# Performance work log

Measured on AMD Instinct MI355X. Metric: run time of the kernel, lower is better.

The kernel has to match this reference:

```python
import jax, jax.numpy as jnp
import numpy as np

B, L, V, D, C, R = 8, 2048, 32000, 512, 64, 64
NBLK = 2           # n_layers - 1
H = 2 * D          # stem hidden dim
STD = 0.02


def _ln(x, w, b):
    m = x.mean(-1, keepdims=True)
    v = ((x - m) ** 2).mean(-1, keepdims=True)
    return (x - m) / jnp.sqrt(v + 1e-5) * w + b


def setup_inputs() -> dict:
    key = jax.random.key(0)
    ks = jax.random.split(key, 16)
    n = lambda k, shp: jax.random.normal(k, shp, dtype=jnp.float32) * STD
    return {
        "token_ids": jax.random.randint(ks[0], (B, L), 0, V),
        "tok_emb": n(ks[1], (V, D)),
        "pos_emb": n(ks[2], (L, D)),
        "stem_ln_w": jnp.ones((NBLK, D), jnp.float32),
        "stem_ln_b": jnp.zeros((NBLK, D), jnp.float32),
        "stem_w1": n(ks[3], (NBLK, D, H)),
        "stem_b1": jnp.zeros((NBLK, H), jnp.float32),
        "stem_w2": n(ks[4], (NBLK, H, D)),
        "stem_b2": jnp.zeros((NBLK, D), jnp.float32),
        "role_ln_w": jnp.ones((D,), jnp.float32),
        "role_ln_b": jnp.zeros((D,), jnp.float32),
        "Wa": n(ks[5], (D, R)),
        "Wb": n(ks[6], (D, R)),
        "Wc": n(ks[7], (D, R)),
        "class_a": n(ks[8], (C, R)),
        "class_b": n(ks[9], (C, R)),
        "class_c": n(ks[10], (C, R)),
        "query_ln_w": jnp.ones((D,), jnp.float32),
        "query_ln_b": jnp.zeros((D,), jnp.float32),
        "Wq": n(ks[11], (D, C)),
        "bq": jnp.zeros((C,), jnp.float32),
    }


def reference(token_ids, tok_emb, pos_emb, stem_ln_w, stem_ln_b, stem_w1,
              stem_b1, stem_w2, stem_b2, role_ln_w, role_ln_b, Wa, Wb, Wc,
              class_a, class_b, class_c, query_ln_w, query_ln_b, Wq, bq):
    seq_len = token_ids.shape[1]
    x = tok_emb[token_ids] + pos_emb[:seq_len][None, :, :]  # [B,L,D]
    for i in range(NBLK):
        h = _ln(x, stem_ln_w[i], stem_ln_b[i])
        h = jax.nn.gelu(h @ stem_w1[i] + stem_b1[i], approximate=False)
        x = x + h @ stem_w2[i] + stem_b2[i]
    prefix = _ln(x[:, :-1], role_ln_w, role_ln_b)  # [B,L-1,D]
    a = jnp.tanh(prefix @ Wa)
    b = jnp.tanh(prefix @ Wb)
    c = jnp.tanh(prefix @ Wc)
    ua = jnp.einsum('blr,cr->blc', a, class_a)  # [B,L-1,C]
    ub = jnp.einsum('blr,cr->blc', b, class_b)
    uc = jnp.einsum('blr,cr->blc', c, class_c)
    # exact ordered-triplet sum  sum_{i<j<k} ua_i * ub_j * uc_k  via exclusive cumsums
    prefA = jnp.cumsum(ua, axis=1) - ua            # sum_{i<j} ua_i
    t = ub * prefA
    prefT = jnp.cumsum(t, axis=1) - t              # sum_{j<k} ub_j * prefA_j
    s = (uc * prefT).sum(axis=1)                   # [B,C]
    Lp = max(seq_len - 1, 1)
    denom = max(Lp * (Lp - 1) * (Lp - 2) / 6.0, 1.0)
    q = _ln(x[:, -1], query_ln_w, query_ln_b)
    return s / denom + q @ Wq + bq
```

## Files before the change

### kernel.cpp

```cpp
#include <hip/hip_runtime.h>

#define NROWS 16384
#define LSEQ  2048
#define NB    8

typedef short v8s __attribute__((ext_vector_type(8)));
typedef float v4f __attribute__((ext_vector_type(4)));

__device__ __forceinline__ unsigned short f2bf(float f) {
    unsigned int u = __float_as_uint(f);
    return (unsigned short)((u + 0x7fffu + ((u >> 16) & 1u)) >> 16);
}
__device__ __forceinline__ float bf2f(unsigned short u) {
    return __uint_as_float(((unsigned int)u) << 16);
}

__device__ __forceinline__ void glds16(const void* g, void* l) {
    __builtin_amdgcn_global_load_lds(
        (__attribute__((address_space(1))) void*)g,
        (__attribute__((address_space(3))) void*)l,
        16, 0, 0);
}

__device__ __forceinline__ float fast_gelu(float v) {
    float z = fabsf(v) * 0.70710678118654752f;
    float t = __builtin_amdgcn_rcpf(1.0f + 0.3275911f * z);
    float poly = t * (0.254829592f + t * (-0.284496736f + t * (1.421413741f +
                 t * (-1.453152027f + t * 1.061405429f))));
    float erfz = 1.0f - poly * __expf(-z * z);
    float er = copysignf(erfz, v);
    return 0.5f * v * (1.0f + er);
}
__device__ __forceinline__ float fast_tanh(float y) {
    float e = __expf(2.0f * y);
    return (e - 1.0f) * __builtin_amdgcn_rcpf(e + 1.0f);
}

__device__ __forceinline__ long swizzled_row(int b, int wave) {
    int T = (b & 7) + (((b >> 3) & 15) << 3);
    int chunk = b >> 7;
    return (long)T * 128 + chunk * 4 + wave;
}

__global__ __launch_bounds__(256) void setup_kernel(
        const int* __restrict__ ids,
        const float* __restrict__ tok, const float* __restrict__ pos,
        const float* __restrict__ g0, const float* __restrict__ b0,
        unsigned short* __restrict__ x, unsigned short* __restrict__ hl,
        const float* __restrict__ w1, const float* __restrict__ w2,
        const float* __restrict__ wa, const float* __restrict__ wb, const float* __restrict__ wc,
        const float* __restrict__ ca, const float* __restrict__ cb, const float* __restrict__ cc,
        unsigned short* __restrict__ w1T, unsigned short* __restrict__ w2T,
        unsigned short* __restrict__ wabcT, unsigned short* __restrict__ clsb) {
    int blk = blockIdx.x;
    int t = threadIdx.x;
    if (blk < 4096) {
        int wave = t >> 6, lane = t & 63;
        long row = swizzled_row(blk, wave);
        int l = (int)(row & (LSEQ - 1));
        int id = ids[row];
        int d = lane * 8;
        float4 t0 = *(const float4*)(tok + (size_t)id * 512 + d);
        float4 t1 = *(const float4*)(tok + (size_t)id * 512 + d + 4);
        float4 p0 = *(const float4*)(pos + (size_t)l * 512 + d);
        float4 p1 = *(const float4*)(pos + (size_t)l * 512 + d + 4);
        float a[8] = {t0.x + p0.x, t0.y + p0.y, t0.z + p0.z, t0.w + p0.w,
                      t1.x + p1.x, t1.y + p1.y, t1.z + p1.z, t1.w + p1.w};
        unsigned int xp[4];
        #pragma unroll
        for (int i = 0; i < 4; ++i)
            xp[i] = (unsigned int)f2bf(a[2 * i]) | ((unsigned int)f2bf(a[2 * i + 1]) << 16);
        *(uint4*)(x + row * 512 + d) = *(uint4*)xp;
        float s = 0.f, s2 = 0.f;
        #pragma unroll
        for (int i = 0; i < 8; ++i) { s += a[i]; s2 += a[i] * a[i]; }
        #pragma unroll
        for (int o = 32; o > 0; o >>= 1) { s += __shfl_down(s, o); s2 += __shfl_down(s2, o); }
        s = __shfl(s, 0); s2 = __shfl(s2, 0);
        float m = s * (1.0f / 512.0f);
        float rinv = 1.0f / sqrtf(s2 * (1.0f / 512.0f) - m * m + 1e-5f);
        float4 ga = *(const float4*)(g0 + d), gb = *(const float4*)(g0 + d + 4);
        float4 ba = *(const float4*)(b0 + d), bb2 = *(const float4*)(b0 + d + 4);
        float gg[8] = {ga.x, ga.y, ga.z, ga.w, gb.x, gb.y, gb.z, gb.w};
        float bb[8] = {ba.x, ba.y, ba.z, ba.w, bb2.x, bb2.y, bb2.z, bb2.w};
        unsigned int hp[4];
        #pragma unroll
        for (int i = 0; i < 4; ++i) {
            unsigned short lo = f2bf((a[2 * i]     - m) * rinv * gg[2 * i]     + bb[2 * i]);
            unsigned short hi = f2bf((a[2 * i + 1] - m) * rinv * gg[2 * i + 1] + bb[2 * i + 1]);
            hp[i] = (unsigned int)lo | ((unsigned int)hi << 16);
        }
        *(uint4*)(hl + row * 512 + d) = *(uint4*)hp;
    } else if (blk < 6240) {
        int id = blk - 4096;
        int tx = t & 31, ty = t >> 5;
        const float* in; unsigned short* out; int R, C, bx, by, ldo;
        if (id < 1024) {
            int l = id >> 9, r = id & 511;
            in = w1 + l * 524288; out = w1T + l * 524288;
            R = 512; C = 1024; bx = r & 31; by = r >> 5; ldo = 512;
        } else if (id < 2048) {
            int l = (id - 1024) >> 9, r = (id - 1024) & 511;
            in = w2 + l * 524288; out = w2T + l * 524288;
            R = 1024; C = 512; bx = r & 15; by = r >> 4; ldo = 1024;
        } else {
            int g = (id - 2048) >> 5, r = (id - 2048) & 31;
            in = (g == 0) ? wa : (g == 1) ? wb : wc;
            out = wabcT + g * 32768;
            R = 512; C = 64; bx = r & 1; by = r >> 1; ldo = 512;
        }
        __shared__ unsigned short tile[32][33];
        int c0 = bx * 32, r0 = by * 32;
        for (int i = ty; i < 32; i += 8) {
            int r = r0 + i, c = c0 + tx;
            tile[i][tx] = (r < R && c < C) ? f2bf(in[(size_t)r * C + c]) : (unsigned short)0;
        }
        __syncthreads();
        for (int i = ty; i < 32; i += 8) {
            int c = c0 + i, r = r0 + tx;
            if (r < R && c < C) out[(size_t)c * ldo + r] = tile[tx][i];
        }
    } else {
        int g = blk - 6240;
        const float* src = (g == 0) ? ca : (g == 1) ? cb : cc;
        unsigned short* dst = clsb + g * 4096;
        for (int i = t; i < 4096; i += 256) dst[i] = f2bf(src[i]);
    }
}

__global__ __launch_bounds__(256) void ln_kernel(const unsigned short* __restrict__ x,
        const float* __restrict__ g, const float* __restrict__ b,
        unsigned short* __restrict__ out) {
    int wave = threadIdx.x >> 6, lane = threadIdx.x & 63;
    long row = swizzled_row(blockIdx.x, wave);
    int d = lane * 8;
    uint4 xp = *(const uint4*)(x + row * 512 + d);
    const unsigned int* xw = (const unsigned int*)&xp;
    float a[8];
    #pragma unroll
    for (int i = 0; i < 4; ++i) {
        a[2 * i]     = bf2f((unsigned short)(xw[i] & 0xffff));
        a[2 * i + 1] = bf2f((unsigned short)(xw[i] >> 16));
    }
    float s = 0.f, s2 = 0.f;
    #pragma unroll
    for (int i = 0; i < 8; ++i) { s += a[i]; s2 += a[i] * a[i]; }
    #pragma unroll
    for (int o = 32; o > 0; o >>= 1) { s += __shfl_down(s, o); s2 += __shfl_down(s2, o); }
    s = __shfl(s, 0); s2 = __shfl(s2, 0);
    float m = s * (1.0f / 512.0f);
    float rinv = 1.0f / sqrtf(s2 * (1.0f / 512.0f) - m * m + 1e-5f);
    float4 g0 = *(const float4*)(g + d), g1 = *(const float4*)(g + d + 4);
    float4 b0 = *(const float4*)(b + d), b1 = *(const float4*)(b + d + 4);
    float gg[8] = {g0.x, g0.y, g0.z, g0.w, g1.x, g1.y, g1.z, g1.w};
    float bb[8] = {b0.x, b0.y, b0.z, b0.w, b1.x, b1.y, b1.z, b1.w};
    unsigned int hp[4];
    #pragma unroll
    for (int i = 0; i < 4; ++i) {
        unsigned short lo = f2bf((a[2 * i]     - m) * rinv * gg[2 * i]     + bb[2 * i]);
        unsigned short hi = f2bf((a[2 * i + 1] - m) * rinv * gg[2 * i + 1] + bb[2 * i + 1]);
        hp[i] = (unsigned int)lo | ((unsigned int)hi << 16);
    }
    *(uint4*)(out + row * 512 + d) = *(uint4*)hp;
}

#define EPI_GELU_BF16  0
#define EPI_RES_BF16   1

template <int EPI, int BN>
__global__ __launch_bounds__(512, 1) void gemm_8p(
        const unsigned short* __restrict__ A, int lda,
        const unsigned short* __restrict__ BT, int ldb,
        const float* __restrict__ bias,
        const unsigned short* __restrict__ xres,
        unsigned short* __restrict__ Cout, int ldc, int K) {
    constexpr int NFC = BN / 64;
    constexpr int FCH = NFC / 2;
    constexpr int NLB = BN / 128;
    constexpr int BH  = BN / 2;
    __shared__ unsigned short Ab[2][2][128 * 64] __attribute__((aligned(16)));
    __shared__ unsigned short Bb[2][2][BH * 64] __attribute__((aligned(16)));
    const int t = threadIdx.x;
    const int lane = t & 63, w = t >> 6;
    const int quad = lane >> 4, l16 = lane & 15;
    const int wmh = w >> 2;
    const int wn  = w & 3;
    const int bhalf = wn >> 1, bbase = (wn & 1) * (BN / 4);
    const long tileM = (long)blockIdx.x * 256;
    const long tileN = (long)blockIdx.y * BN;

    const int rl = lane >> 3;
    const int cl = ((lane & 7) ^ rl) * 8;

    const unsigned short* pa[2][2];
    #pragma unroll
    for (int h = 0; h < 2; ++h)
        #pragma unroll
        for (int q = 0; q < 2; ++q)
            pa[h][q] = A + (tileM + h * 128 + w * 16 + q * 8 + rl) * (size_t)lda + cl;
    const unsigned short* pb[2][2];
    #pragma unroll
    for (int h = 0; h < 2; ++h) {
        if constexpr (NLB == 2) {
            #pragma unroll
            for (int q = 0; q < 2; ++q)
                pb[h][q] = BT + (tileN + h * BH + w * 16 + q * 8 + rl) * (size_t)ldb + cl;
        } else {
            pb[h][0] = BT + (tileN + h * BH + w * 8 + rl) * (size_t)ldb + cl;
        }
    }
    int kA = 0, kB = 0;

    auto stageA = [&](int buf, int h) {
        glds16(pa[h][0] + kA, &Ab[buf][h][(w * 2 + 0) * 512]);
        glds16(pa[h][1] + kA, &Ab[buf][h][(w * 2 + 1) * 512]);
    };
    auto stageB = [&](int buf, int h) {
        if constexpr (NLB == 2) {
            glds16(pb[h][0] + kB, &Bb[buf][h][(w * 2 + 0) * 512]);
            glds16(pb[h][1] + kB, &Bb[buf][h][(w * 2 + 1) * 512]);
        } else {
            glds16(pb[h][0] + kB, &Bb[buf][h][w * 512]);
        }
    };

    const int xl = l16 & 7;
    const int ak0 = l16 * 64 + (((quad    ) ^ xl) * 8);
    const int ak1 = l16 * 64 + (((quad + 4) ^ xl) * 8);

    stageA(0, 0); stageA(0, 1); kA = 64;
    stageB(0, 0); stageB(0, 1); kB = 64;
    stageB(1, 0); stageB(1, 1); kB = 128;

    v4f acc[8][NFC] = {};
    const int nt = K >> 6;

    asm volatile("s_waitcnt vmcnt(%0)" :: "i"(2 * NLB) : "memory");
    __builtin_amdgcn_s_barrier();

    for (int tt = 0; tt < nt; ++tt) {
        const int bi = tt & 1;
        const unsigned short* Ah = &Ab[bi][wmh][0];
        const unsigned short* Bh = &Bb[bi][bhalf][bbase * 64];
        v8s af[4][2], bf[NFC][2];

        #pragma unroll
        for (int fr = 0; fr < 4; ++fr) {
            af[fr][0] = *(const v8s*)(Ah + fr * 1024 + ak0);
            af[fr][1] = *(const v8s*)(Ah + fr * 1024 + ak1);
        }
        #pragma unroll
        for (int fc = 0; fc < FCH; ++fc) {
            bf[fc][0] = *(const v8s*)(Bh + fc * 1024 + ak0);
            bf[fc][1] = *(const v8s*)(Bh + fc * 1024 + ak1);
        }
        if (tt + 1 < nt) stageA(bi ^ 1, 0);
        __builtin_amdgcn_s_barrier();
        asm volatile("s_waitcnt lgkmcnt(0)" ::: "memory");
        __builtin_amdgcn_s_setprio(1);
        #pragma unroll
        for (int fr = 0; fr < 4; ++fr)
            #pragma unroll
            for (int fc = 0; fc < FCH; ++fc) {
                acc[fr][fc] = __builtin_amdgcn_mfma_f32_16x16x32_bf16(bf[fc][0], af[fr][0], acc[fr][fc], 0, 0, 0);
                acc[fr][fc] = __builtin_amdgcn_mfma_f32_16x16x32_bf16(bf[fc][1], af[fr][1], acc[fr][fc], 0, 0, 0);
            }
        __builtin_amdgcn_s_setprio(0);
        __builtin_amdgcn_s_barrier();

        #pragma unroll
        for (int fc = FCH; fc < NFC; ++fc) {
            bf[fc][0] = *(const v8s*)(Bh + fc * 1024 + ak0);
            bf[fc][1] = *(const v8s*)(Bh + fc * 1024 + ak1);
        }
        if (tt + 1 < nt) stageA(bi ^ 1, 1);
        kA += 64;
        __builtin_amdgcn_s_barrier();
        asm volatile("s_waitcnt lgkmcnt(0)" ::: "memory");
        __builtin_amdgcn_s_setprio(1);
        #pragma unroll
        for (int fr = 0; fr < 4; ++fr)
            #pragma unroll
            for (int fc = FCH; fc < NFC; ++fc) {
                acc[fr][fc] = __builtin_amdgcn_mfma_f32_16x16x32_bf16(bf[fc][0], af[fr][0], acc[fr][fc], 0, 0, 0);
                acc[fr][fc] = __builtin_amdgcn_mfma_f32_16x16x32_bf16(bf[fc][1], af[fr][1], acc[fr][fc], 0, 0, 0);
            }
        __builtin_amdgcn_s_setprio(0);
        __builtin_amdgcn_s_barrier();

        #pragma unroll
        for (int fr = 0; fr < 4; ++fr) {
            af[fr][0] = *(const v8s*)(Ah + (fr + 4) * 1024 + ak0);
            af[fr][1] = *(const v8s*)(Ah + (fr + 4) * 1024 + ak1);
        }
        if (tt + 2 < nt) stageB(bi, 0);
        __builtin_amdgcn_s_barrier();
        asm volatile("s_waitcnt lgkmcnt(0)" ::: "memory");
        __builtin_amdgcn_s_setprio(1);
        #pragma unroll
        for (int fr = 0; fr < 4; ++fr)
            #pragma unroll
            for (int fc = 0; fc < FCH; ++fc) {
                acc[fr + 4][fc] = __builtin_amdgcn_mfma_f32_16x16x32_bf16(bf[fc][0], af[fr][0], acc[fr + 4][fc], 0, 0, 0);
                acc[fr + 4][fc] = __builtin_amdgcn_mfma_f32_16x16x32_bf16(bf[fc][1], af[fr][1], acc[fr + 4][fc], 0, 0, 0);
            }
        __builtin_amdgcn_s_setprio(0);
        __builtin_amdgcn_s_barrier();

        if (tt + 2 < nt) stageB(bi, 1);
        kB += 64;
        if (tt + 2 < nt)
            asm volatile("s_waitcnt vmcnt(%0)" :: "i"(2 * NLB) : "memory");
        else if (tt + 1 < nt)
            asm volatile("s_waitcnt vmcnt(0)" ::: "memory");
        __builtin_amdgcn_s_barrier();
        __builtin_amdgcn_s_setprio(1);
        #pragma unroll
        for (int fr = 0; fr < 4; ++fr)
            #pragma unroll
            for (int fc = FCH; fc < NFC; ++fc) {
                acc[fr + 4][fc] = __builtin_amdgcn_mfma_f32_16x16x32_bf16(bf[fc][0], af[fr][0], acc[fr + 4][fc], 0, 0, 0);
                acc[fr + 4][fc] = __builtin_amdgcn_mfma_f32_16x16x32_bf16(bf[fc][1], af[fr][1], acc[fr + 4][fc], 0, 0, 0);
            }
        __builtin_amdgcn_s_setprio(0);
        __builtin_amdgcn_s_barrier();
    }

    #pragma unroll
    for (int fr = 0; fr < 8; ++fr) {
        long m = tileM + wmh * 128 + fr * 16 + l16;
        #pragma unroll
        for (int fc = 0; fc < NFC; ++fc) {
            long n0 = tileN + wn * (BN / 4) + fc * 16 + quad * 4;
            float4 bi4 = *(const float4*)&bias[n0];
            const float* bip = (const float*)&bi4;
            unsigned short pk[4];
            if (EPI == EPI_GELU_BF16) {
                #pragma unroll
                for (int r = 0; r < 4; ++r)
                    pk[r] = f2bf(fast_gelu(acc[fr][fc][r] + bip[r]));
            } else {
                ushort4 xr4 = *(const ushort4*)&xres[m * ldc + n0];
                const unsigned short* xp = (const unsigned short*)&xr4;
                #pragma unroll
                for (int r = 0; r < 4; ++r)
                    pk[r] = f2bf(acc[fr][fc][r] + bip[r] + bf2f(xp[r]));
            }
            *(ushort4*)&Cout[m * ldc + n0] = *(ushort4*)pk;
        }
    }
}

__global__ __launch_bounds__(256) void tanh_class_kernel(
        const unsigned short* __restrict__ A,
        const unsigned short* __restrict__ WT,
        const unsigned short* __restrict__ cls,
        unsigned short* __restrict__ uu) {
    __shared__ unsigned short As[128][40] __attribute__((aligned(16)));
    __shared__ unsigned short Bs[64][40] __attribute__((aligned(16)));
    __shared__ unsigned short P[128 * 72] __attribute__((aligned(16)));
    const int t = threadIdx.x;
    const int lane = t & 63, wave = t >> 6;
    const int quad = lane >> 4, l16 = lane & 15;
    const int wm = (wave >> 1) * 64, wn = (wave & 1) * 32;
    const long tileM = (long)blockIdx.x * 128;
    const int g = blockIdx.y;
    const int arow = t >> 2, acol = (t & 3) * 8;

    const unsigned short* BT = WT + g * 32768;
    v8s cf[2][2];
    #pragma unroll
    for (int ks = 0; ks < 2; ++ks)
        #pragma unroll
        for (int j = 0; j < 2; ++j)
            cf[ks][j] = *(const v8s*)&cls[g * 4096 + (wn + j * 16 + l16) * 64 + ks * 32 + quad * 8];

    const unsigned short* gA0 = A + (tileM + arow) * 512 + acol;
    const unsigned short* gA1 = gA0 + 64 * 512;
    const unsigned short* gB0 = BT + arow * 512 + acol;

    v4f acc[4][2] = {};
    uint4 a0, a1, b0;
    a0 = *(const uint4*)gA0; a1 = *(const uint4*)gA1; gA0 += 32; gA1 += 32;
    b0 = *(const uint4*)gB0; gB0 += 32;
    *(uint4*)&As[arow][acol] = a0;
    *(uint4*)&As[arow + 64][acol] = a1;
    *(uint4*)&Bs[arow][acol] = b0;

    for (int kk = 0; kk < 16; ++kk) {
        __syncthreads();
        const bool more = kk < 15;
        if (more) {
            a0 = *(const uint4*)gA0; a1 = *(const uint4*)gA1; gA0 += 32; gA1 += 32;
            b0 = *(const uint4*)gB0; gB0 += 32;
        }
        v8s af[4], bfr[2];
        #pragma unroll
        for (int i = 0; i < 4; ++i) af[i] = *(const v8s*)&As[wm + i * 16 + l16][quad * 8];
        #pragma unroll
        for (int j = 0; j < 2; ++j) bfr[j] = *(const v8s*)&Bs[wn + j * 16 + l16][quad * 8];
        #pragma unroll
        for (int i = 0; i < 4; ++i)
            #pragma unroll
            for (int j = 0; j < 2; ++j)
                acc[i][j] = __builtin_amdgcn_mfma_f32_16x16x32_bf16(bfr[j], af[i], acc[i][j], 0, 0, 0);
        __syncthreads();
        if (more) {
            *(uint4*)&As[arow][acol] = a0;
            *(uint4*)&As[arow + 64][acol] = a1;
            *(uint4*)&Bs[arow][acol] = b0;
        }
    }

    #pragma unroll
    for (int i = 0; i < 4; ++i) {
        int m = wm + i * 16 + l16;
        #pragma unroll
        for (int j = 0; j < 2; ++j) {
            int n0 = wn + j * 16 + quad * 4;
            unsigned short pk[4];
            #pragma unroll
            for (int r = 0; r < 4; ++r) pk[r] = f2bf(fast_tanh(acc[i][j][r]));
            *(ushort4*)&P[m * 72 + n0] = *(ushort4*)pk;
        }
    }
    __syncthreads();

    v4f acc2[4][2] = {};
    #pragma unroll
    for (int ks = 0; ks < 2; ++ks) {
        v8s paf[4];
        #pragma unroll
        for (int i = 0; i < 4; ++i)
            paf[i] = *(const v8s*)&P[(wm + i * 16 + l16) * 72 + ks * 32 + quad * 8];
        #pragma unroll
        for (int i = 0; i < 4; ++i)
            #pragma unroll
            for (int j = 0; j < 2; ++j)
                acc2[i][j] = __builtin_amdgcn_mfma_f32_16x16x32_bf16(cf[ks][j], paf[i], acc2[i][j], 0, 0, 0);
    }

    #pragma unroll
    for (int i = 0; i < 4; ++i) {
        long m = tileM + wm + i * 16 + l16;
        #pragma unroll
        for (int j = 0; j < 2; ++j) {
            int c0 = wn + j * 16 + quad * 4;
            unsigned short pk[4];
            #pragma unroll
            for (int r = 0; r < 4; ++r) pk[r] = f2bf(acc2[i][j][r]);
            *(ushort4*)&uu[m * 192 + g * 64 + c0] = *(ushort4*)pk;
        }
    }
}

__global__ __launch_bounds__(64) void scan_part_kernel(const unsigned short* __restrict__ u,
                                                       float* __restrict__ part) {
    int b = blockIdx.x, seg = blockIdx.y;
    int c = threadIdx.x;
    int l0 = seg * 32;
    int l1 = l0 + 32; if (l1 > 2047) l1 = 2047;
    float sA = 0.f, sB = 0.f, sC = 0.f, T = 0.f, M = 0.f, U = 0.f;
    const unsigned short* base = u + ((size_t)b * LSEQ + l0) * 192 + c;
    for (int l = l0; l < l1; ++l) {
        float ua = bf2f(base[0]), ub = bf2f(base[64]), uc = bf2f(base[128]);
        base += 192;
        U += uc * T;
        M += uc * sB;
        T += ub * sA;
        sA += ua; sB += ub; sC += uc;
    }
    float* p = part + ((size_t)(b * 64 + seg)) * 384 + c;
    p[0] = sA; p[64] = sB; p[128] = sC; p[192] = T; p[256] = M; p[320] = U;
}

__global__ __launch_bounds__(64) void combine_final_kernel(const float* __restrict__ part,
        const unsigned short* __restrict__ x,
        const float* __restrict__ qw, const float* __restrict__ qb,
        const float* __restrict__ Wq, const float* __restrict__ bq,
        float* __restrict__ out, float inv_denom) {
    int b = blockIdx.x;
    int c = threadIdx.x;
    const float* p = part + (size_t)b * 64 * 384 + c;
    float A = p[0], B = p[64], Tt = p[192], Mt = p[256], Ut = p[320];
    for (int seg = 1; seg < 64; ++seg) {
        const float* q2 = p + seg * 384;
        float a2 = q2[0], b2 = q2[64], c2 = q2[128], t2 = q2[192], m2 = q2[256], u2 = q2[320];
        float Un = Ut + u2 + c2 * Tt + A * m2;
        float Tn = Tt + t2 + A * b2;
        float Mn = Mt + m2 + B * c2;
        A += a2; B += b2;
        Ut = Un; Tt = Tn; Mt = Mn;
    }
    __shared__ float q[512];
    __shared__ float mv[2];
    const unsigned short* xr = x + ((size_t)b * LSEQ + (LSEQ - 1)) * 512;
    float s1 = 0.f, s2 = 0.f;
    for (int i = c; i < 512; i += 64) { float v = bf2f(xr[i]); q[i] = v; s1 += v; s2 += v * v; }
    #pragma unroll
    for (int o = 32; o > 0; o >>= 1) { s1 += __shfl_down(s1, o); s2 += __shfl_down(s2, o); }
    if (c == 0) {
        float m = s1 * (1.0f / 512.0f);
        float var = s2 * (1.0f / 512.0f) - m * m;
        mv[0] = m; mv[1] = 1.0f / sqrtf(var + 1e-5f);
    }
    __syncthreads();
    float m = mv[0], r = mv[1];
    for (int i = c; i < 512; i += 64) q[i] = (q[i] - m) * r * qw[i] + qb[i];
    __syncthreads();
    float acc = 0.f;
    for (int d = 0; d < 512; ++d) acc += q[d] * Wq[d * 64 + c];
    out[b * 64 + c] = Ut * inv_denom + acc + bq[c];
}

extern "C" void kernel_launch(void* const* d_in, const int* in_sizes, int n_in,
                              void* d_out, int out_size, void* d_ws, size_t ws_size,
                              hipStream_t stream) {
    const int*   token_ids   = (const int*)d_in[0];
    const float* tok_emb     = (const float*)d_in[1];
    const float* pos_emb     = (const float*)d_in[2];
    const float* stem_ln_w   = (const float*)d_in[3];
    const float* stem_ln_b   = (const float*)d_in[4];
    const float* stem_w1     = (const float*)d_in[5];
    const float* stem_b1     = (const float*)d_in[6];
    const float* stem_w2     = (const float*)d_in[7];
    const float* stem_b2     = (const float*)d_in[8];
    const float* role_ln_w   = (const float*)d_in[9];
    const float* role_ln_b   = (const float*)d_in[10];
    const float* Wa          = (const float*)d_in[11];
    const float* Wb          = (const float*)d_in[12];
    const float* Wc          = (const float*)d_in[13];
    const float* class_a     = (const float*)d_in[14];
    const float* class_b     = (const float*)d_in[15];
    const float* class_c     = (const float*)d_in[16];
    const float* query_ln_w  = (const float*)d_in[17];
    const float* query_ln_b  = (const float*)d_in[18];
    const float* Wq          = (const float*)d_in[19];
    const float* bq          = (const float*)d_in[20];
    float* out = (float*)d_out;

    char* wsb = (char*)d_ws;
    unsigned short* x    = (unsigned short*)(wsb);
    unsigned short* hl   = (unsigned short*)(wsb + 16777216);
    unsigned short* Hb   = (unsigned short*)(wsb + 33554432);
    unsigned short* uu   = (unsigned short*)(wsb + 67108864);
    float* part          = (float*)(wsb + 73400320);
    unsigned short* w1T  = (unsigned short*)(wsb + 74188800);
    unsigned short* w2T  = (unsigned short*)(wsb + 76285952);
    unsigned short* wabcT= (unsigned short*)(wsb + 78383104);
    unsigned short* clsb = (unsigned short*)(wsb + 78579712);

    setup_kernel<<<6243, 256, 0, stream>>>(token_ids, tok_emb, pos_emb,
        stem_ln_w, stem_ln_b, x, hl,
        stem_w1, stem_w2, Wa, Wb, Wc, class_a, class_b, class_c,
        w1T, w2T, wabcT, clsb);

    for (int i = 0; i < 2; ++i) {
        if (i > 0)
            ln_kernel<<<NROWS / 4, 256, 0, stream>>>(x, stem_ln_w + 512, stem_ln_b + 512, hl);
        gemm_8p<EPI_GELU_BF16, 256><<<dim3(64, 4), 512, 0, stream>>>(
            hl, 512, w1T + i * 524288, 512, stem_b1 + i * 1024, nullptr, Hb, 1024, 512);
        gemm_8p<EPI_RES_BF16, 128><<<dim3(64, 4), 512, 0, stream>>>(
            Hb, 1024, w2T + i * 524288, 1024, stem_b2 + i * 512, x, x, 512, 1024);
    }

    ln_kernel<<<NROWS / 4, 256, 0, stream>>>(x, role_ln_w, role_ln_b, hl);

    tanh_class_kernel<<<dim3(128, 3), 256, 0, stream>>>(hl, wabcT, clsb, uu);

    scan_part_kernel<<<dim3(NB, 64), 64, 0, stream>>>(uu, part);

    float inv_denom = (float)(6.0 / (2047.0 * 2046.0 * 2045.0));
    combine_final_kernel<<<NB, 64, 0, stream>>>(part, x, query_ln_w, query_ln_b,
                                                Wq, bq, out, inv_denom);
}
```

Baseline: 327.1 us.

## Fuse second stem GEMM with residual add and following LayerNorm

```diff
diff --git a/kernel.cpp b/kernel.cpp
--- a/kernel.cpp
+++ b/kernel.cpp
@@ -128,44 +128,7 @@
     }
 }
 
-__global__ __launch_bounds__(256) void ln_kernel(const unsigned short* __restrict__ x,
-        const float* __restrict__ g, const float* __restrict__ b,
-        unsigned short* __restrict__ out) {
-    int wave = threadIdx.x >> 6, lane = threadIdx.x & 63;
-    long row = swizzled_row(blockIdx.x, wave);
-    int d = lane * 8;
-    uint4 xp = *(const uint4*)(x + row * 512 + d);
-    const unsigned int* xw = (const unsigned int*)&xp;
-    float a[8];
-    #pragma unroll
-    for (int i = 0; i < 4; ++i) {
-        a[2 * i]     = bf2f((unsigned short)(xw[i] & 0xffff));
-        a[2 * i + 1] = bf2f((unsigned short)(xw[i] >> 16));
-    }
-    float s = 0.f, s2 = 0.f;
-    #pragma unroll
-    for (int i = 0; i < 8; ++i) { s += a[i]; s2 += a[i] * a[i]; }
-    #pragma unroll
-    for (int o = 32; o > 0; o >>= 1) { s += __shfl_down(s, o); s2 += __shfl_down(s2, o); }
-    s = __shfl(s, 0); s2 = __shfl(s2, 0);
-    float m = s * (1.0f / 512.0f);
-    float rinv = 1.0f / sqrtf(s2 * (1.0f / 512.0f) - m * m + 1e-5f);
-    float4 g0 = *(const float4*)(g + d), g1 = *(const float4*)(g + d + 4);
-    float4 b0 = *(const float4*)(b + d), b1 = *(const float4*)(b + d + 4);
-    float gg[8] = {g0.x, g0.y, g0.z, g0.w, g1.x, g1.y, g1.z, g1.w};
-    float bb[8] = {b0.x, b0.y, b0.z, b0.w, b1.x, b1.y, b1.z, b1.w};
-    unsigned int hp[4];
-    #pragma unroll
-    for (int i = 0; i < 4; ++i) {
-        unsigned short lo = f2bf((a[2 * i]     - m) * rinv * gg[2 * i]     + bb[2 * i]);
-        unsigned short hi = f2bf((a[2 * i + 1] - m) * rinv * gg[2 * i + 1] + bb[2 * i + 1]);
-        hp[i] = (unsigned int)lo | ((unsigned int)hi << 16);
-    }
-    *(uint4*)(out + row * 512 + d) = *(uint4*)hp;
-}
-
 #define EPI_GELU_BF16  0
-#define EPI_RES_BF16   1
 
 template <int EPI, int BN>
 __global__ __launch_bounds__(512, 1) void gemm_8p(
@@ -335,18 +298,135 @@
             float4 bi4 = *(const float4*)&bias[n0];
             const float* bip = (const float*)&bi4;
             unsigned short pk[4];
-            if (EPI == EPI_GELU_BF16) {
-                #pragma unroll
-                for (int r = 0; r < 4; ++r)
-                    pk[r] = f2bf(fast_gelu(acc[fr][fc][r] + bip[r]));
-            } else {
-                ushort4 xr4 = *(const ushort4*)&xres[m * ldc + n0];
-                const unsigned short* xp = (const unsigned short*)&xr4;
-                #pragma unroll
-                for (int r = 0; r < 4; ++r)
-                    pk[r] = f2bf(acc[fr][fc][r] + bip[r] + bf2f(xp[r]));
+            #pragma unroll
+            for (int r = 0; r < 4; ++r)
+                pk[r] = f2bf(fast_gelu(acc[fr][fc][r] + bip[r]));
+            *(ushort4*)&Cout[m * ldc + n0] = *(ushort4*)pk;
+        }
+    }
+}
+
+__global__ __launch_bounds__(512) void gemm_w2ln(
+        const unsigned short* __restrict__ A,
+        const unsigned short* __restrict__ BT,
+        const float* __restrict__ bias,
+        unsigned short* __restrict__ x,
+        const float* __restrict__ lnw, const float* __restrict__ lnb,
+        unsigned short* __restrict__ hl) {
+    constexpr int NT = 32;
+    __shared__ unsigned short As[2][64 * 32] __attribute__((aligned(16)));
+    __shared__ unsigned short Bs[2][512 * 32] __attribute__((aligned(16)));
+    __shared__ float sbuf[64][4];
+    __shared__ float s2buf[64][4];
+    const int t = threadIdx.x;
+    const int lane = t & 63, w = t >> 6;
+    const int quad = lane >> 4, l16 = lane & 15;
+    const int wm = (w >> 2) * 32;
+    const int wnq = w & 3;
+    const int wn = wnq * 128;
+    const long tileM = (long)blockIdx.x * 64;
+
+    const int lr = lane >> 2, lc = (lane & 3) * 8;
+    const unsigned short* gA = A + (tileM + (w & 3) * 16 + lr) * 1024 + lc;
+    const unsigned short* gB[4];
+    #pragma unroll
+    for (int q = 0; q < 4; ++q)
+        gB[q] = BT + (w * 64 + q * 16 + lr) * 1024 + lc;
+    int koff = 0;
+
+    auto stage = [&](int buf) {
+        if (w < 4) glds16(gA + koff, &As[buf][w * 512]);
+        #pragma unroll
+        for (int q = 0; q < 4; ++q)
+            glds16(gB[q] + koff, &Bs[buf][(w * 4 + q) * 512]);
+        koff += 32;
+    };
+
+    v4f acc[2][8] = {};
+    stage(0);
+    int cur = 0;
+    for (int kk = 0; kk < NT; ++kk) {
+        if (kk + 1 < NT) {
+            stage(cur ^ 1);
+            if (w < 4) asm volatile("s_waitcnt vmcnt(5)" ::: "memory");
+            else       asm volatile("s_waitcnt vmcnt(4)" ::: "memory");
+        } else {
+            asm volatile("s_waitcnt vmcnt(0)" ::: "memory");
+        }
+        asm volatile("s_barrier" ::: "memory");
+        v8s af[2], bfr[8];
+        #pragma unroll
+        for (int i = 0; i < 2; ++i)
+            af[i] = *(const v8s*)&As[cur][(wm + i * 16 + l16) * 32 + quad * 8];
+        #pragma unroll
+        for (int j = 0; j < 8; ++j)
+            bfr[j] = *(const v8s*)&Bs[cur][(wn + j * 16 + l16) * 32 + quad * 8];
+        #pragma unroll
+        for (int i = 0; i < 2; ++i)
+            #pragma unroll
+            for (int j = 0; j < 8; ++j)
+                acc[i][j] = __builtin_amdgcn_mfma_f32_16x16x32_bf16(bfr[j], af[i], acc[i][j], 0, 0, 0);
+        if (kk + 1 < NT)
+            asm volatile("s_barrier" ::: "memory");
+        cur ^= 1;
+    }
+
+    float s1v[2] = {0.f, 0.f}, s2v[2] = {0.f, 0.f};
+    #pragma unroll
+    for (int i = 0; i < 2; ++i) {
+        long m = tileM + wm + i * 16 + l16;
+        #pragma unroll
+        for (int j = 0; j < 8; ++j) {
+            int n0 = wn + j * 16 + quad * 4;
+            float4 bi4 = *(const float4*)&bias[n0];
+            const float* bip = (const float*)&bi4;
+            ushort4 xr4 = *(const ushort4*)&x[m * 512 + n0];
+            const unsigned short* xp = (const unsigned short*)&xr4;
+            unsigned short pk[4];
+            #pragma unroll
+            for (int r = 0; r < 4; ++r) {
+                float v = acc[i][j][r] + bip[r] + bf2f(xp[r]);
+                acc[i][j][r] = v;
+                s1v[i] += v; s2v[i] += v * v;
+                pk[r] = f2bf(v);
             }
-            *(ushort4*)&Cout[m * ldc + n0] = *(ushort4*)pk;
+            *(ushort4*)&x[m * 512 + n0] = *(ushort4*)pk;
+        }
+    }
+    #pragma unroll
+    for (int i = 0; i < 2; ++i) {
+        s1v[i] += __shfl_xor(s1v[i], 16); s1v[i] += __shfl_xor(s1v[i], 32);
+        s2v[i] += __shfl_xor(s2v[i], 16); s2v[i] += __shfl_xor(s2v[i], 32);
+    }
+    if (quad == 0) {
+        #pragma unroll
+        for (int i = 0; i < 2; ++i) {
+            int r = wm + i * 16 + l16;
+            sbuf[r][wnq] = s1v[i];
+            s2buf[r][wnq] = s2v[i];
+        }
+    }
+    __syncthreads();
+    #pragma unroll
+    for (int i = 0; i < 2; ++i) {
+        int r = wm + i * 16 + l16;
+        long m = tileM + r;
+        float s1 = sbuf[r][0] + sbuf[r][1] + sbuf[r][2] + sbuf[r][3];
+        float s2 = s2buf[r][0] + s2buf[r][1] + s2buf[r][2] + s2buf[r][3];
+        float mean = s1 * (1.0f / 512.0f);
+        float rinv = 1.0f / sqrtf(s2 * (1.0f / 512.0f) - mean * mean + 1e-5f);
+        #pragma unroll
+        for (int j = 0; j < 8; ++j) {
+            int n0 = wn + j * 16 + quad * 4;
+            float4 g4 = *(const float4*)&lnw[n0];
+            float4 b4 = *(const float4*)&lnb[n0];
+            const float* gp = (const float*)&g4;
+            const float* bp = (const float*)&b4;
+            unsigned short pk[4];
+            #pragma unroll
+            for (int r2 = 0; r2 < 4; ++r2)
+                pk[r2] = f2bf((acc[i][j][r2] - mean) * rinv * gp[r2] + bp[r2]);
+            *(ushort4*)&hl[m * 512 + n0] = *(ushort4*)pk;
         }
     }
 }
@@ -556,15 +636,14 @@
         w1T, w2T, wabcT, clsb);
 
     for (int i = 0; i < 2; ++i) {
-        if (i > 0)
-            ln_kernel<<<NROWS / 4, 256, 0, stream>>>(x, stem_ln_w + 512, stem_ln_b + 512, hl);
         gemm_8p<EPI_GELU_BF16, 256><<<dim3(64, 4), 512, 0, stream>>>(
             hl, 512, w1T + i * 524288, 512, stem_b1 + i * 1024, nullptr, Hb, 1024, 512);
-        gemm_8p<EPI_RES_BF16, 128><<<dim3(64, 4), 512, 0, stream>>>(
-            Hb, 1024, w2T + i * 524288, 1024, stem_b2 + i * 512, x, x, 512, 1024);
-    }
-
-    ln_kernel<<<NROWS / 4, 256, 0, stream>>>(x, role_ln_w, role_ln_b, hl);
+        gemm_w2ln<<<256, 512, 0, stream>>>(
+            Hb, w2T + i * 524288, stem_b2 + i * 512, x,
+            (i == 0) ? stem_ln_w + 512 : role_ln_w,
+            (i == 0) ? stem_ln_b + 512 : role_ln_b,
+            hl);
+    }
 
     tanh_class_kernel<<<dim3(128, 3), 256, 0, stream>>>(hl, wabcT, clsb, uu);
 
```

Measured after the change: 351.8 us. 1.08x slower.

## Fold LayerNorm into following GEMMs via row statistics and precomputed weight sums

Applied to the files above, without the earlier changes.

```diff
diff --git a/kernel.cpp b/kernel.cpp
--- a/kernel.cpp
+++ b/kernel.cpp
@@ -46,12 +46,16 @@
         const int* __restrict__ ids,
         const float* __restrict__ tok, const float* __restrict__ pos,
         const float* __restrict__ g0, const float* __restrict__ b0,
-        unsigned short* __restrict__ x, unsigned short* __restrict__ hl,
+        const float* __restrict__ rolew, const float* __restrict__ roleb,
+        const float* __restrict__ b1all,
+        unsigned short* __restrict__ x, float* __restrict__ rowstat0,
         const float* __restrict__ w1, const float* __restrict__ w2,
         const float* __restrict__ wa, const float* __restrict__ wb, const float* __restrict__ wc,
         const float* __restrict__ ca, const float* __restrict__ cb, const float* __restrict__ cc,
         unsigned short* __restrict__ w1T, unsigned short* __restrict__ w2T,
-        unsigned short* __restrict__ wabcT, unsigned short* __restrict__ clsb) {
+        unsigned short* __restrict__ wabcT, unsigned short* __restrict__ clsb,
+        float* __restrict__ c1buf, float* __restrict__ c2buf,
+        float* __restrict__ c1a, float* __restrict__ c2a) {
     int blk = blockIdx.x;
     int t = threadIdx.x;
     if (blk < 4096) {
@@ -76,29 +80,20 @@
         for (int i = 0; i < 8; ++i) { s += a[i]; s2 += a[i] * a[i]; }
         #pragma unroll
         for (int o = 32; o > 0; o >>= 1) { s += __shfl_down(s, o); s2 += __shfl_down(s2, o); }
-        s = __shfl(s, 0); s2 = __shfl(s2, 0);
-        float m = s * (1.0f / 512.0f);
-        float rinv = 1.0f / sqrtf(s2 * (1.0f / 512.0f) - m * m + 1e-5f);
-        float4 ga = *(const float4*)(g0 + d), gb = *(const float4*)(g0 + d + 4);
-        float4 ba = *(const float4*)(b0 + d), bb2 = *(const float4*)(b0 + d + 4);
-        float gg[8] = {ga.x, ga.y, ga.z, ga.w, gb.x, gb.y, gb.z, gb.w};
-        float bb[8] = {ba.x, ba.y, ba.z, ba.w, bb2.x, bb2.y, bb2.z, bb2.w};
-        unsigned int hp[4];
-        #pragma unroll
-        for (int i = 0; i < 4; ++i) {
-            unsigned short lo = f2bf((a[2 * i]     - m) * rinv * gg[2 * i]     + bb[2 * i]);
-            unsigned short hi = f2bf((a[2 * i + 1] - m) * rinv * gg[2 * i + 1] + bb[2 * i + 1]);
-            hp[i] = (unsigned int)lo | ((unsigned int)hi << 16);
-        }
-        *(uint4*)(hl + row * 512 + d) = *(uint4*)hp;
+        if (lane == 0) {
+            rowstat0[row * 2] = s;
+            rowstat0[row * 2 + 1] = s2;
+        }
     } else if (blk < 6240) {
         int id = blk - 4096;
         int tx = t & 31, ty = t >> 5;
         const float* in; unsigned short* out; int R, C, bx, by, ldo;
+        const float* gfold = nullptr;
         if (id < 1024) {
             int l = id >> 9, r = id & 511;
             in = w1 + l * 524288; out = w1T + l * 524288;
             R = 512; C = 1024; bx = r & 31; by = r >> 5; ldo = 512;
+            gfold = g0 + l * 512;
         } else if (id < 2048) {
             int l = (id - 1024) >> 9, r = (id - 1024) & 511;
             in = w2 + l * 524288; out = w2T + l * 524288;
@@ -108,76 +103,66 @@
             in = (g == 0) ? wa : (g == 1) ? wb : wc;
             out = wabcT + g * 32768;
             R = 512; C = 64; bx = r & 1; by = r >> 1; ldo = 512;
+            gfold = rolew;
         }
         __shared__ unsigned short tile[32][33];
         int c0 = bx * 32, r0 = by * 32;
         for (int i = ty; i < 32; i += 8) {
             int r = r0 + i, c = c0 + tx;
-            tile[i][tx] = (r < R && c < C) ? f2bf(in[(size_t)r * C + c]) : (unsigned short)0;
+            float v = (r < R && c < C) ? in[(size_t)r * C + c] : 0.f;
+            if (gfold && r < R) v *= gfold[r];
+            tile[i][tx] = f2bf(v);
         }
         __syncthreads();
         for (int i = ty; i < 32; i += 8) {
             int c = c0 + i, r = r0 + tx;
             if (r < R && c < C) out[(size_t)c * ldo + r] = tile[tx][i];
         }
-    } else {
+    } else if (blk < 6243) {
         int g = blk - 6240;
         const float* src = (g == 0) ? ca : (g == 1) ? cb : cc;
         unsigned short* dst = clsb + g * 4096;
         for (int i = t; i < 4096; i += 256) dst[i] = f2bf(src[i]);
-    }
-}
-
-__global__ __launch_bounds__(256) void ln_kernel(const unsigned short* __restrict__ x,
-        const float* __restrict__ g, const float* __restrict__ b,
-        unsigned short* __restrict__ out) {
-    int wave = threadIdx.x >> 6, lane = threadIdx.x & 63;
-    long row = swizzled_row(blockIdx.x, wave);
-    int d = lane * 8;
-    uint4 xp = *(const uint4*)(x + row * 512 + d);
-    const unsigned int* xw = (const unsigned int*)&xp;
-    float a[8];
-    #pragma unroll
-    for (int i = 0; i < 4; ++i) {
-        a[2 * i]     = bf2f((unsigned short)(xw[i] & 0xffff));
-        a[2 * i + 1] = bf2f((unsigned short)(xw[i] >> 16));
-    }
-    float s = 0.f, s2 = 0.f;
-    #pragma unroll
-    for (int i = 0; i < 8; ++i) { s += a[i]; s2 += a[i] * a[i]; }
-    #pragma unroll
-    for (int o = 32; o > 0; o >>= 1) { s += __shfl_down(s, o); s2 += __shfl_down(s2, o); }
-    s = __shfl(s, 0); s2 = __shfl(s2, 0);
-    float m = s * (1.0f / 512.0f);
-    float rinv = 1.0f / sqrtf(s2 * (1.0f / 512.0f) - m * m + 1e-5f);
-    float4 g0 = *(const float4*)(g + d), g1 = *(const float4*)(g + d + 4);
-    float4 b0 = *(const float4*)(b + d), b1 = *(const float4*)(b + d + 4);
-    float gg[8] = {g0.x, g0.y, g0.z, g0.w, g1.x, g1.y, g1.z, g1.w};
-    float bb[8] = {b0.x, b0.y, b0.z, b0.w, b1.x, b1.y, b1.z, b1.w};
-    unsigned int hp[4];
-    #pragma unroll
-    for (int i = 0; i < 4; ++i) {
-        unsigned short lo = f2bf((a[2 * i]     - m) * rinv * gg[2 * i]     + bb[2 * i]);
-        unsigned short hi = f2bf((a[2 * i + 1] - m) * rinv * gg[2 * i + 1] + bb[2 * i + 1]);
-        hp[i] = (unsigned int)lo | ((unsigned int)hi << 16);
-    }
-    *(uint4*)(out + row * 512 + d) = *(uint4*)hp;
-}
-
-#define EPI_GELU_BF16  0
-#define EPI_RES_BF16   1
-
-template <int EPI, int BN>
-__global__ __launch_bounds__(512, 1) void gemm_8p(
-        const unsigned short* __restrict__ A, int lda,
-        const unsigned short* __restrict__ BT, int ldb,
-        const float* __restrict__ bias,
-        const unsigned short* __restrict__ xres,
-        unsigned short* __restrict__ Cout, int ldc, int K) {
-    constexpr int NFC = BN / 64;
-    constexpr int FCH = NFC / 2;
-    constexpr int NLB = BN / 128;
-    constexpr int BH  = BN / 2;
+    } else if (blk < 6251) {
+        int c = blk - 6243;
+        int l = c >> 2, nb = c & 3;
+        int n = nb * 256 + t;
+        const float* W = w1 + l * 524288;
+        const float* g = g0 + l * 512;
+        const float* b = b0 + l * 512;
+        float a1 = 0.f, a2 = 0.f;
+        for (int k = 0; k < 512; ++k) {
+            float w = W[(size_t)k * 1024 + n];
+            a1 += g[k] * w;
+            a2 += b[k] * w;
+        }
+        c1buf[l * 1024 + n] = a1;
+        c2buf[l * 1024 + n] = a2 + b1all[l * 1024 + n];
+    } else {
+        if (t < 192) {
+            int gi = t >> 6, r = t & 63;
+            const float* W = (gi == 0) ? wa : (gi == 1) ? wb : wc;
+            float a1 = 0.f, a2 = 0.f;
+            for (int k = 0; k < 512; ++k) {
+                float w = W[(size_t)k * 64 + r];
+                a1 += rolew[k] * w;
+                a2 += roleb[k] * w;
+            }
+            c1a[t] = a1;
+            c2a[t] = a2;
+        }
+    }
+}
+
+template <int SM>
+__global__ __launch_bounds__(512, 1) void gemm_w1(
+        const unsigned short* __restrict__ A,
+        const unsigned short* __restrict__ BT,
+        const float* __restrict__ c1, const float* __restrict__ c2,
+        const float* __restrict__ stats,
+        unsigned short* __restrict__ Cout) {
+    constexpr int BN = 256, NFC = 4, FCH = 2, NLB = 2, BH = 128;
+    constexpr int lda = 512, ldb = 512, ldc = 1024, K = 512;
     __shared__ unsigned short Ab[2][2][128 * 64] __attribute__((aligned(16)));
     __shared__ unsigned short Bb[2][2][BH * 64] __attribute__((aligned(16)));
     const int t = threadIdx.x;
@@ -200,15 +185,10 @@
             pa[h][q] = A + (tileM + h * 128 + w * 16 + q * 8 + rl) * (size_t)lda + cl;
     const unsigned short* pb[2][2];
     #pragma unroll
-    for (int h = 0; h < 2; ++h) {
-        if constexpr (NLB == 2) {
-            #pragma unroll
-            for (int q = 0; q < 2; ++q)
-                pb[h][q] = BT + (tileN + h * BH + w * 16 + q * 8 + rl) * (size_t)ldb + cl;
-        } else {
-            pb[h][0] = BT + (tileN + h * BH + w * 8 + rl) * (size_t)ldb + cl;
-        }
-    }
+    for (int h = 0; h < 2; ++h)
+        #pragma unroll
+        for (int q = 0; q < 2; ++q)
+            pb[h][q] = BT + (tileN + h * BH + w * 16 + q * 8 + rl) * (size_t)ldb + cl;
     int kA = 0, kB = 0;
 
     auto stageA = [&](int buf, int h) {
@@ -216,12 +196,8 @@
         glds16(pa[h][1] + kA, &Ab[buf][h][(w * 2 + 1) * 512]);
     };
     auto stageB = [&](int buf, int h) {
-        if constexpr (NLB == 2) {
-            glds16(pb[h][0] + kB, &Bb[buf][h][(w * 2 + 0) * 512]);
-            glds16(pb[h][1] + kB, &Bb[buf][h][(w * 2 + 1) * 512]);
-        } else {
-            glds16(pb[h][0] + kB, &Bb[buf][h][w * 512]);
-        }
+        glds16(pb[h][0] + kB, &Bb[buf][h][(w * 2 + 0) * 512]);
+        glds16(pb[h][1] + kB, &Bb[buf][h][(w * 2 + 1) * 512]);
     };
 
     const int xl = l16 & 7;
@@ -329,25 +305,225 @@
     #pragma unroll
     for (int fr = 0; fr < 8; ++fr) {
         long m = tileM + wmh * 128 + fr * 16 + l16;
+        float s1, s2;
+        if (SM == 0) {
+            float2 st = *(const float2*)&stats[m * 2];
+            s1 = st.x; s2 = st.y;
+        } else {
+            float4 q0 = *(const float4*)&stats[m * 8];
+            float4 q1 = *(const float4*)&stats[m * 8 + 4];
+            s1 = q0.x + q0.z + q1.x + q1.z;
+            s2 = q0.y + q0.w + q1.y + q1.w;
+        }
+        float mu = s1 * (1.0f / 512.0f);
+        float rinv = 1.0f / sqrtf(s2 * (1.0f / 512.0f) - mu * mu + 1e-5f);
+        float rmu = rinv * mu;
         #pragma unroll
         for (int fc = 0; fc < NFC; ++fc) {
             long n0 = tileN + wn * (BN / 4) + fc * 16 + quad * 4;
-            float4 bi4 = *(const float4*)&bias[n0];
+            float4 c14 = *(const float4*)&c1[n0];
+            float4 c24 = *(const float4*)&c2[n0];
+            const float* c1p = (const float*)&c14;
+            const float* c2p = (const float*)&c24;
+            unsigned short pk[4];
+            #pragma unroll
+            for (int r = 0; r < 4; ++r)
+                pk[r] = f2bf(fast_gelu(rinv * acc[fr][fc][r] - rmu * c1p[r] + c2p[r]));
+            *(ushort4*)&Cout[m * ldc + n0] = *(ushort4*)pk;
+        }
+    }
+}
+
+__global__ __launch_bounds__(512, 1) void gemm_w2(
+        const unsigned short* __restrict__ A,
+        const unsigned short* __restrict__ BT,
+        const float* __restrict__ bias,
+        unsigned short* __restrict__ x,
+        float* __restrict__ rowpart) {
+    constexpr int BN = 128, NFC = 2, FCH = 1, NLB = 1, BH = 64;
+    constexpr int lda = 1024, ldb = 1024, K = 1024;
+    __shared__ unsigned short Ab[2][2][128 * 64] __attribute__((aligned(16)));
+    __shared__ unsigned short Bb[2][2][BH * 64] __attribute__((aligned(16)));
+    const int t = threadIdx.x;
+    const int lane = t & 63, w = t >> 6;
+    const int quad = lane >> 4, l16 = lane & 15;
+    const int wmh = w >> 2;
+    const int wn  = w & 3;
+    const int bhalf = wn >> 1, bbase = (wn & 1) * (BN / 4);
+    const long tileM = (long)blockIdx.x * 256;
+    const int yb = blockIdx.y;
+    const long tileN = (long)yb * BN;
+
+    const int rl = lane >> 3;
+    const int cl = ((lane & 7) ^ rl) * 8;
+
+    const unsigned short* pa[2][2];
+    #pragma unroll
+    for (int h = 0; h < 2; ++h)
+        #pragma unroll
+        for (int q = 0; q < 2; ++q)
+            pa[h][q] = A + (tileM + h * 128 + w * 16 + q * 8 + rl) * (size_t)lda + cl;
+    const unsigned short* pb[2];
+    #pragma unroll
+    for (int h = 0; h < 2; ++h)
+        pb[h] = BT + (tileN + h * BH + w * 8 + rl) * (size_t)ldb + cl;
+    int kA = 0, kB = 0;
+
+    auto stageA = [&](int buf, int h) {
+        glds16(pa[h][0] + kA, &Ab[buf][h][(w * 2 + 0) * 512]);
+        glds16(pa[h][1] + kA, &Ab[buf][h][(w * 2 + 1) * 512]);
+    };
+    auto stageB = [&](int buf, int h) {
+        glds16(pb[h] + kB, &Bb[buf][h][w * 512]);
+    };
+
+    const int xl = l16 & 7;
+    const int ak0 = l16 * 64 + (((quad    ) ^ xl) * 8);
+    const int ak1 = l16 * 64 + (((quad + 4) ^ xl) * 8);
+
+    stageA(0, 0); stageA(0, 1); kA = 64;
+    stageB(0, 0); stageB(0, 1); kB = 64;
+    stageB(1, 0); stageB(1, 1); kB = 128;
+
+    v4f acc[8][NFC] = {};
+    const int nt = K >> 6;
+
+    asm volatile("s_waitcnt vmcnt(%0)" :: "i"(2 * NLB) : "memory");
+    __builtin_amdgcn_s_barrier();
+
+    for (int tt = 0; tt < nt; ++tt) {
+        const int bi = tt & 1;
+        const unsigned short* Ah = &Ab[bi][wmh][0];
+        const unsigned short* Bh = &Bb[bi][bhalf][bbase * 64];
+        v8s af[4][2], bf[NFC][2];
+
+        #pragma unroll
+        for (int fr = 0; fr < 4; ++fr) {
+            af[fr][0] = *(const v8s*)(Ah + fr * 1024 + ak0);
+            af[fr][1] = *(const v8s*)(Ah + fr * 1024 + ak1);
+        }
+        #pragma unroll
+        for (int fc = 0; fc < FCH; ++fc) {
+            bf[fc][0] = *(const v8s*)(Bh + fc * 1024 + ak0);
+            bf[fc][1] = *(const v8s*)(Bh + fc * 1024 + ak1);
+        }
+        if (tt + 1 < nt) stageA(bi ^ 1, 0);
+        __builtin_amdgcn_s_barrier();
+        asm volatile("s_waitcnt lgkmcnt(0)" ::: "memory");
+        __builtin_amdgcn_s_setprio(1);
+        #pragma unroll
+        for (int fr = 0; fr < 4; ++fr)
+            #pragma unroll
+            for (int fc = 0; fc < FCH; ++fc) {
+                acc[fr][fc] = __builtin_amdgcn_mfma_f32_16x16x32_bf16(bf[fc][0], af[fr][0], acc[fr][fc], 0, 0, 0);
+                acc[fr][fc] = __builtin_amdgcn_mfma_f32_16x16x32_bf16(bf[fc][1], af[fr][1], acc[fr][fc], 0, 0, 0);
+            }
+        __builtin_amdgcn_s_setprio(0);
+        __builtin_amdgcn_s_barrier();
+
+        #pragma unroll
+        for (int fc = FCH; fc < NFC; ++fc) {
+            bf[fc][0] = *(const v8s*)(Bh + fc * 1024 + ak0);
+            bf[fc][1] = *(const v8s*)(Bh + fc * 1024 + ak1);
+        }
+        if (tt + 1 < nt) stageA(bi ^ 1, 1);
+        kA += 64;
+        __builtin_amdgcn_s_barrier();
+        asm volatile("s_waitcnt lgkmcnt(0)" ::: "memory");
+        __builtin_amdgcn_s_setprio(1);
+        #pragma unroll
+        for (int fr = 0; fr < 4; ++fr)
+            #pragma unroll
+            for (int fc = FCH; fc < NFC; ++fc) {
+                acc[fr][fc] = __builtin_amdgcn_mfma_f32_16x16x32_bf16(bf[fc][0], af[fr][0], acc[fr][fc], 0, 0, 0);
+                acc[fr][fc] = __builtin_amdgcn_mfma_f32_16x16x32_bf16(bf[fc][1], af[fr][1], acc[fr][fc], 0, 0, 0);
+            }
+        __builtin_amdgcn_s_setprio(0);
+        __builtin_amdgcn_s_barrier();
+
+        #pragma unroll
+        for (int fr = 0; fr < 4; ++fr) {
+            af[fr][0] = *(const v8s*)(Ah + (fr + 4) * 1024 + ak0);
+            af[fr][1] = *(const v8s*)(Ah + (fr + 4) * 1024 + ak1);
+        }
+        if (tt + 2 < nt) stageB(bi, 0);
+        __builtin_amdgcn_s_barrier();
+        asm volatile("s_waitcnt lgkmcnt(0)" ::: "memory");
+        __builtin_amdgcn_s_setprio(1);
+        #pragma unroll
+        for (int fr = 0; fr < 4; ++fr)
+            #pragma unroll
+            for (int fc = 0; fc < FCH; ++fc) {
+                acc[fr + 4][fc] = __builtin_amdgcn_mfma_f32_16x16x32_bf16(bf[fc][0], af[fr][0], acc[fr + 4][fc], 0, 0, 0);
+                acc[fr + 4][fc] = __builtin_amdgcn_mfma_f32_16x16x32_bf16(bf[fc][1], af[fr][1], acc[fr + 4][fc], 0, 0, 0);
+            }
+        __builtin_amdgcn_s_setprio(0);
+        __builtin_amdgcn_s_barrier();
+
+        if (tt + 2 < nt) stageB(bi, 1);
+        kB += 64;
+        if (tt + 2 < nt)
+            asm volatile("s_waitcnt vmcnt(%0)" :: "i"(2 * NLB) : "memory");
+        else if (tt + 1 < nt)
+            asm volatile("s_waitcnt vmcnt(0)" ::: "memory");
+        __builtin_amdgcn_s_barrier();
+        __builtin_amdgcn_s_setprio(1);
+        #pragma unroll
+        for (int fr = 0; fr < 4; ++fr)
+            #pragma unroll
+            for (int fc = FCH; fc < NFC; ++fc) {
+                acc[fr + 4][fc] = __builtin_amdgcn_mfma_f32_16x16x32_bf16(bf[fc][0], af[fr][0], acc[fr + 4][fc], 0, 0, 0);
+                acc[fr + 4][fc] = __builtin_amdgcn_mfma_f32_16x16x32_bf16(bf[fc][1], af[fr][1], acc[fr + 4][fc], 0, 0, 0);
+            }
+        __builtin_amdgcn_s_setprio(0);
+        __builtin_amdgcn_s_barrier();
+    }
+
+    float p1[8], p2[8];
+    #pragma unroll
+    for (int fr = 0; fr < 8; ++fr) { p1[fr] = 0.f; p2[fr] = 0.f; }
+    #pragma unroll
+    for (int fr = 0; fr < 8; ++fr) {
+        long m = tileM + wmh * 128 + fr * 16 + l16;
+        #pragma unroll
+        for (int fc = 0; fc < NFC; ++fc) {
+            long n0 = tileN + wn * (BN / 4) + fc * 16 + quad * 4;
+            float4 bi4 = *(const float4*)&bias[n0 - tileN + yb * BN];
             const float* bip = (const float*)&bi4;
+            ushort4 xr4 = *(const ushort4*)&x[m * 512 + n0];
+            const unsigned short* xp = (const unsigned short*)&xr4;
             unsigned short pk[4];
-            if (EPI == EPI_GELU_BF16) {
-                #pragma unroll
-                for (int r = 0; r < 4; ++r)
-                    pk[r] = f2bf(fast_gelu(acc[fr][fc][r] + bip[r]));
-            } else {
-                ushort4 xr4 = *(const ushort4*)&xres[m * ldc + n0];
-                const unsigned short* xp = (const unsigned short*)&xr4;
-                #pragma unroll
-                for (int r = 0; r < 4; ++r)
-                    pk[r] = f2bf(acc[fr][fc][r] + bip[r] + bf2f(xp[r]));
-            }
-            *(ushort4*)&Cout[m * ldc + n0] = *(ushort4*)pk;
-        }
+            #pragma unroll
+            for (int r = 0; r < 4; ++r) {
+                float v = acc[fr][fc][r] + bip[r] + bf2f(xp[r]);
+                p1[fr] += v; p2[fr] += v * v;
+                pk[r] = f2bf(v);
+            }
+            *(ushort4*)&x[m * 512 + n0] = *(ushort4*)pk;
+        }
+    }
+    #pragma unroll
+    for (int fr = 0; fr < 8; ++fr) {
+        p1[fr] += __shfl_xor(p1[fr], 16); p1[fr] += __shfl_xor(p1[fr], 32);
+        p2[fr] += __shfl_xor(p2[fr], 16); p2[fr] += __shfl_xor(p2[fr], 32);
+    }
+    float* red = (float*)&Ab[0][0][0];
+    if (quad == 0) {
+        #pragma unroll
+        for (int fr = 0; fr < 8; ++fr) {
+            int r = wmh * 128 + fr * 16 + l16;
+            red[r * 4 + wn] = p1[fr];
+            red[1024 + r * 4 + wn] = p2[fr];
+        }
+    }
+    __syncthreads();
+    if (t < 256) {
+        int r = t;
+        float s1 = red[r * 4] + red[r * 4 + 1] + red[r * 4 + 2] + red[r * 4 + 3];
+        float s2 = red[1024 + r * 4] + red[1024 + r * 4 + 1] + red[1024 + r * 4 + 2] + red[1024 + r * 4 + 3];
+        long m = tileM + r;
+        rowpart[m * 8 + yb * 2]     = s1;
+        rowpart[m * 8 + yb * 2 + 1] = s2;
     }
 }
 
@@ -355,6 +531,8 @@
         const unsigned short* __restrict__ A,
         const unsigned short* __restrict__ WT,
         const unsigned short* __restrict__ cls,
+        const float* __restrict__ rowpart,
+        const float* __restrict__ c1a, const float* __restrict__ c2a,
         unsigned short* __restrict__ uu) {
     __shared__ unsigned short As[128][40] __attribute__((aligned(16)));
     __shared__ unsigned short Bs[64][40] __attribute__((aligned(16)));
@@ -415,12 +593,25 @@
     #pragma unroll
     for (int i = 0; i < 4; ++i) {
         int m = wm + i * 16 + l16;
+        long gm = tileM + m;
+        float4 q0 = *(const float4*)&rowpart[gm * 8];
+        float4 q1 = *(const float4*)&rowpart[gm * 8 + 4];
+        float s1 = q0.x + q0.z + q1.x + q1.z;
+        float s2 = q0.y + q0.w + q1.y + q1.w;
+        float mu = s1 * (1.0f / 512.0f);
+        float rinv = 1.0f / sqrtf(s2 * (1.0f / 512.0f) - mu * mu + 1e-5f);
+        float rmu = rinv * mu;
         #pragma unroll
         for (int j = 0; j < 2; ++j) {
             int n0 = wn + j * 16 + quad * 4;
+            float4 c14 = *(const float4*)&c1a[g * 64 + n0];
+            float4 c24 = *(const float4*)&c2a[g * 64 + n0];
+            const float* c1p = (const float*)&c14;
+            const float* c2p = (const float*)&c24;
             unsigned short pk[4];
             #pragma unroll
-            for (int r = 0; r < 4; ++r) pk[r] = f2bf(fast_tanh(acc[i][j][r]));
+            for (int r = 0; r < 4; ++r)
+                pk[r] = f2bf(fast_tanh(rinv * acc[i][j][r] - rmu * c1p[r] + c2p[r]));
             *(ushort4*)&P[m * 72 + n0] = *(ushort4*)pk;
         }
     }
@@ -541,32 +732,38 @@
 
     char* wsb = (char*)d_ws;
     unsigned short* x    = (unsigned short*)(wsb);
-    unsigned short* hl   = (unsigned short*)(wsb + 16777216);
-    unsigned short* Hb   = (unsigned short*)(wsb + 33554432);
-    unsigned short* uu   = (unsigned short*)(wsb + 67108864);
-    float* part          = (float*)(wsb + 73400320);
-    unsigned short* w1T  = (unsigned short*)(wsb + 74188800);
-    unsigned short* w2T  = (unsigned short*)(wsb + 76285952);
-    unsigned short* wabcT= (unsigned short*)(wsb + 78383104);
-    unsigned short* clsb = (unsigned short*)(wsb + 78579712);
-
-    setup_kernel<<<6243, 256, 0, stream>>>(token_ids, tok_emb, pos_emb,
-        stem_ln_w, stem_ln_b, x, hl,
+    unsigned short* Hb   = (unsigned short*)(wsb + 16777216);
+    unsigned short* uu   = (unsigned short*)(wsb + 50331648);
+    float* part          = (float*)(wsb + 56623104);
+    unsigned short* w1T  = (unsigned short*)(wsb + 57409536);
+    unsigned short* w2T  = (unsigned short*)(wsb + 59506688);
+    unsigned short* wabcT= (unsigned short*)(wsb + 61603840);
+    unsigned short* clsb = (unsigned short*)(wsb + 61800448);
+    float* rowstat0      = (float*)(wsb + 61825024);
+    float* rowpart1      = (float*)(wsb + 61956096);
+    float* rowpart2      = (float*)(wsb + 62480384);
+    float* c1buf         = (float*)(wsb + 63004672);
+    float* c2buf         = (float*)(wsb + 63012864);
+    float* c1a           = (float*)(wsb + 63021056);
+    float* c2a           = (float*)(wsb + 63021824);
+
+    setup_kernel<<<6252, 256, 0, stream>>>(token_ids, tok_emb, pos_emb,
+        stem_ln_w, stem_ln_b, role_ln_w, role_ln_b, stem_b1,
+        x, rowstat0,
         stem_w1, stem_w2, Wa, Wb, Wc, class_a, class_b, class_c,
-        w1T, w2T, wabcT, clsb);
-
-    for (int i = 0; i < 2; ++i) {
-        if (i > 0)
-            ln_kernel<<<NROWS / 4, 256, 0, stream>>>(x, stem_ln_w + 512, stem_ln_b + 512, hl);
-        gemm_8p<EPI_GELU_BF16, 256><<<dim3(64, 4), 512, 0, stream>>>(
-            hl, 512, w1T + i * 524288, 512, stem_b1 + i * 1024, nullptr, Hb, 1024, 512);
-        gemm_8p<EPI_RES_BF16, 128><<<dim3(64, 4), 512, 0, stream>>>(
-            Hb, 1024, w2T + i * 524288, 1024, stem_b2 + i * 512, x, x, 512, 1024);
-    }
-
-    ln_kernel<<<NROWS / 4, 256, 0, stream>>>(x, role_ln_w, role_ln_b, hl);
-
-    tanh_class_kernel<<<dim3(128, 3), 256, 0, stream>>>(hl, wabcT, clsb, uu);
+        w1T, w2T, wabcT, clsb, c1buf, c2buf, c1a, c2a);
+
+    gemm_w1<0><<<dim3(64, 4), 512, 0, stream>>>(
+        x, w1T, c1buf, c2buf, rowstat0, Hb);
+    gemm_w2<<<dim3(64, 4), 512, 0, stream>>>(
+        Hb, w2T, stem_b2, x, rowpart1);
+    gemm_w1<1><<<dim3(64, 4), 512, 0, stream>>>(
+        x, w1T + 524288, c1buf + 1024, c2buf + 1024, rowpart1, Hb);
+    gemm_w2<<<dim3(64, 4), 512, 0, stream>>>(
+        Hb, w2T + 524288, stem_b2 + 512, x, rowpart2);
+
+    tanh_class_kernel<<<dim3(128, 3), 256, 0, stream>>>(x, wabcT, clsb,
+                                                        rowpart2, c1a, c2a, uu);
 
     scan_part_kernel<<<dim3(NB, 64), 64, 0, stream>>>(uu, part);
 
```

After: 346.6 us. 6.0% more time.
